# Kernel tuning notes

Hardware: AMD Instinct MI355X
Metric: run time of the kernel (lower is better)

## Reference

```python
import jax, jax.numpy as jnp
import numpy as np

KERNEL = 8


def setup_inputs() -> dict:
    key = jax.random.key(0)
    ks = jax.random.split(key, 9)
    N, Cin, L = 16, 128, 2048
    Cout = 256
    x = jax.random.normal(ks[0], (N, Cin, L), dtype=jnp.float32)
    conv_w = jax.random.normal(ks[1], (Cout, Cin, KERNEL), dtype=jnp.float32) * (1.0 / np.sqrt(Cin * KERNEL))
    conv_b = jax.random.normal(ks[2], (Cout,), dtype=jnp.float32) * 0.01
    wq = jax.random.normal(ks[3], (Cout, Cout), dtype=jnp.float32) * (1.0 / np.sqrt(Cout))
    bq = jax.random.normal(ks[4], (Cout,), dtype=jnp.float32) * 0.01
    wk = jax.random.normal(ks[5], (Cout, Cout), dtype=jnp.float32) * (1.0 / np.sqrt(Cout))
    bk = jax.random.normal(ks[6], (Cout,), dtype=jnp.float32) * 0.01
    wv = jax.random.normal(ks[7], (Cout, Cout), dtype=jnp.float32) * (1.0 / np.sqrt(Cout))
    bv = jax.random.normal(ks[8], (Cout,), dtype=jnp.float32) * 0.01
    return {"x": x, "conv_w": conv_w, "conv_b": conv_b,
            "wq": wq, "bq": bq, "wk": wk, "bk": bk, "wv": wv, "bv": bv}


def reference(x, conv_w, conv_b, wq, bq, wk, bk, wv, bv):
    # Conv1d, valid padding: [N, Cin, L] -> [N, Cout, S], S = L - KERNEL + 1
    h = jax.lax.conv_general_dilated(
        x, conv_w, window_strides=(1,), padding='VALID',
        dimension_numbers=('NCH', 'OIH', 'NCH'))
    h = jax.nn.relu(h + conv_b[None, :, None])
    N, C, S = h.shape
    h = jnp.transpose(h, (0, 2, 1))  # [N, S, C]
    # Linear layers (torch convention: y = x @ W^T + b)
    q = jnp.einsum('nsc,dc->nsd', h, wq) + bq
    k = jnp.einsum('nsc,dc->nsd', h, wk) + bk
    v = jnp.einsum('nsc,dc->nsd', h, wv) + bv
    # sigmoid (non-normalized) attention over full SxS scores
    scores = jnp.einsum('nsd,ntd->nst', q, k) / jnp.sqrt(jnp.asarray(C, h.dtype))
    attn = jax.nn.sigmoid(scores)  # [N, S, S]
    out = jnp.einsum('nst,ntd->nsd', attn, v)
    return jnp.transpose(out, (0, 2, 1))  # [N, C, S]
```

## Files before the change

kernel.cpp:

```cpp
#include <hip/hip_runtime.h>

typedef short short8 __attribute__((ext_vector_type(8)));
typedef float f32x4 __attribute__((ext_vector_type(4)));
typedef float f32x16 __attribute__((ext_vector_type(16)));
typedef unsigned short u16x4 __attribute__((ext_vector_type(4)));

constexpr int NB = 16, CIN = 128, LIN = 2048, CO = 256;
constexpr int SL = 2041;
constexpr int MP = 32768;
constexpr int XTS = 136;
constexpr int QSTR = 2048 * CO + 256;


constexpr size_t XT_OFF = 0;
constexpr size_t XT_SZ  = (size_t)NB*LIN*XTS*2 + 65536;
constexpr size_t CW_OFF = XT_OFF + XT_SZ;
constexpr size_t CW_SZ  = (size_t)CO*CIN*8*2;
constexpr size_t WQ_OFF = CW_OFF + CW_SZ;
constexpr size_t WB_SZ  = (size_t)CO*CO*2;
constexpr size_t WK_OFF = WQ_OFF + WB_SZ;
constexpr size_t WV_OFF = WK_OFF + WB_SZ;
constexpr size_t Q_OFF  = WV_OFF + WB_SZ;
constexpr size_t QK_SZ  = (size_t)NB*QSTR*2 + 256;
constexpr size_t K_OFF  = Q_OFF + QK_SZ;
constexpr size_t VT_OFF = K_OFF + QK_SZ;

__device__ inline unsigned short f2bf(float f) {
  union { float f; unsigned int u; } v; v.f = f;
  unsigned int r = v.u + 0x7fffu + ((v.u >> 16) & 1u);
  return (unsigned short)(r >> 16);
}

__device__ inline void sync_lds() {
  __asm__ volatile("" ::: "memory");
  __builtin_amdgcn_s_waitcnt(0xc07f);
  __builtin_amdgcn_s_barrier();
  __asm__ volatile("" ::: "memory");
}
__device__ inline void barrier_only() {
  __asm__ volatile("" ::: "memory");
  __builtin_amdgcn_s_barrier();
  __asm__ volatile("" ::: "memory");
}

#if defined(__has_builtin)
#if __has_builtin(__builtin_amdgcn_global_load_lds)
#define HAVE_GLDS 1
#endif
#endif

__device__ inline void gld16(const unsigned short* g, void* l) {
#ifdef HAVE_GLDS
  __builtin_amdgcn_global_load_lds(
      (const __attribute__((address_space(1))) void*)g,
      (__attribute__((address_space(3))) void*)l, 16, 0, 0);
#else
  *(short8*)l = *(const short8*)g;
#endif
}

__global__ __launch_bounds__(256) void prep_kernel(
    const float* __restrict__ x, unsigned short* __restrict__ xt,
    const float* __restrict__ cw_in, unsigned short* __restrict__ cw_out,
    const float* __restrict__ wq, const float* __restrict__ wk, const float* __restrict__ wv,
    unsigned short* __restrict__ wqb, unsigned short* __restrict__ wkb,
    unsigned short* __restrict__ wvb) {
  __shared__ float tile[32][33];
  const int b = blockIdx.x;
  const int tid = threadIdx.x;
  if (b < 4096) {
    const int tx = tid & 31, ty = tid >> 5;
    const int s0 = (b & 63) * 32, c0 = ((b >> 6) & 3) * 32, n = b >> 8;
    #pragma unroll
    for (int r = 0; r < 4; ++r)
      tile[ty * 4 + r][tx] = x[((size_t)(n * CIN + c0 + ty * 4 + r)) * LIN + s0 + tx];
    __syncthreads();
    #pragma unroll
    for (int r = 0; r < 4; ++r)
      xt[((size_t)(n * LIN + s0 + ty * 4 + r)) * XTS + c0 + tx] = f2bf(tile[tx][ty * 4 + r]);
  } else if (b < 4096 + 1024) {
    int idx = (b - 4096) * 256 + tid;
    int co = idx >> 10, r = idx & 1023, kp = r >> 7, ci = r & 127;
    cw_out[idx] = f2bf(cw_in[co * 1024 + ci * 8 + kp]);
  } else {
    int lb2 = b - (4096 + 1024);
    int z = lb2 >> 6, lb = lb2 & 63;
    const float* src = (z == 0) ? wq : (z == 1) ? wk : wv;
    unsigned short* dst = (z == 0) ? wqb : (z == 1) ? wkb : wvb;
    int i = (lb * 256 + tid) * 4;
    float4 v = *(const float4*)(src + i);
    u16x4 r;
    r.x = f2bf(v.x); r.y = f2bf(v.y); r.z = f2bf(v.z); r.w = f2bf(v.w);
    *(u16x4*)(dst + i) = r;
  }
}

__global__ __launch_bounds__(256, 2) void conv_qkv(
    const unsigned short* __restrict__ xt,
    const unsigned short* __restrict__ wb,
    const float* __restrict__ cbias,
    const unsigned short* __restrict__ Bq, const unsigned short* __restrict__ Bk,
    const unsigned short* __restrict__ Bv,
    const float* __restrict__ biq, const float* __restrict__ bik,
    const float* __restrict__ biv,
    unsigned short* __restrict__ qb, unsigned short* __restrict__ kb,
    unsigned short* __restrict__ vtb)
{
  __shared__ unsigned short regA[16384];
  __shared__ unsigned short sB[2][8192];
  unsigned short* const sX = regA;
  unsigned short* const hL = regA;
  const int tid = threadIdx.x;
  const int w = tid >> 6, lane = tid & 63, quad = lane >> 4, l16 = lane & 15;
  const int sg = w >> 1, dh = w & 1;
  const int n = blockIdx.y, s0 = blockIdx.x * 64;

  {
    const unsigned short* xbase = xt + ((size_t)n * LIN + s0) * XTS;
    #pragma unroll
    for (int i = 0; i < 5; ++i) {
      int u = i * 256 + tid;
      if (u < 1207) gld16(xbase + u * 8, ((char*)sX) + u * 16);
    }
  }

  const int brow0 = tid >> 2, bkgs = tid & 3;
  short8 breg[4];
  #pragma unroll
  for (int i2 = 0; i2 < 4; ++i2) {
    int row = i2 * 64 + brow0;
    int kg = bkgs ^ ((row >> 1) & 3);
    breg[i2] = *(const short8*)(wb + (size_t)row * 1024 + kg * 8);
  }
  #pragma unroll
  for (int i2 = 0; i2 < 4; ++i2)
    *(short8*)(&sB[0][(i2 * 256 + tid) * 8]) = breg[i2];
  __syncthreads();

  f32x4 acc[2][8];
  #pragma unroll
  for (int i = 0; i < 2; ++i)
    #pragma unroll
    for (int j = 0; j < 8; ++j) acc[i][j] = (f32x4){0.f, 0.f, 0.f, 0.f};

  for (int kc = 0; kc < 32; ++kc) {
    const int kcn = (kc < 31) ? kc + 1 : kc;
    const int kpn = kcn >> 2, ci0n = (kcn & 3) * 32;
    #pragma unroll
    for (int i2 = 0; i2 < 4; ++i2) {
      int row = i2 * 64 + brow0;
      int kg = bkgs ^ ((row >> 1) & 3);
      breg[i2] = *(const short8*)(wb + (size_t)row * 1024 + kpn * 128 + ci0n + kg * 8);
    }

    const int kp = kc >> 2, ci0 = (kc & 3) * 32;
    const unsigned short* sBc = sB[kc & 1];
    short8 bfr[8];
    #pragma unroll
    for (int j = 0; j < 8; ++j) {
      int r = dh * 128 + j * 16 + l16;
      bfr[j] = *(const short8*)(sBc + r * 32 + (quad ^ ((r >> 1) & 3)) * 8);
    }
    #pragma unroll
    for (int i = 0; i < 2; ++i) {
      int srow = sg * 32 + i * 16 + l16;
      short8 afr = *(const short8*)(sX + (srow + kp) * XTS + ci0 + quad * 8);
      #pragma unroll
      for (int j = 0; j < 8; ++j)
        acc[i][j] = __builtin_amdgcn_mfma_f32_16x16x32_bf16(afr, bfr[j], acc[i][j], 0, 0, 0);
    }

    #pragma unroll
    for (int i2 = 0; i2 < 4; ++i2)
      *(short8*)(&sB[(kc + 1) & 1][(i2 * 256 + tid) * 8]) = breg[i2];
    sync_lds();
  }

  #pragma unroll
  for (int i = 0; i < 2; ++i)
    #pragma unroll
    for (int j = 0; j < 8; ++j) {
      int c = dh * 128 + j * 16 + l16;
      float bv = cbias[c];
      int cc = (c >> 5) * 32 + (c & 7);
      int g = (c >> 3) & 3;
      #pragma unroll
      for (int jj = 0; jj < 4; ++jj) {
        int r = sg * 32 + i * 16 + quad * 4 + jj;
        hL[r * 256 + cc + ((g ^ ((r >> 1) & 3)) << 3)] =
            f2bf(fmaxf(acc[i][j][jj] + bv, 0.f));
      }
    }

  for (int z = 0; z < 3; ++z) {
    const unsigned short* B = (z == 0) ? Bq : (z == 1) ? Bk : Bv;
    const float* bias        = (z == 0) ? biq : (z == 1) ? bik : biv;

    #pragma unroll
    for (int i2 = 0; i2 < 4; ++i2) {
      int row = i2 * 64 + brow0;
      int kg = bkgs ^ ((row >> 1) & 3);
      breg[i2] = *(const short8*)(B + (size_t)row * CO + kg * 8);
    }
    #pragma unroll
    for (int i2 = 0; i2 < 4; ++i2)
      *(short8*)(&sB[0][(i2 * 256 + tid) * 8]) = breg[i2];
    sync_lds();

    #pragma unroll
    for (int i = 0; i < 2; ++i)
      #pragma unroll
      for (int j = 0; j < 8; ++j) acc[i][j] = (f32x4){0.f, 0.f, 0.f, 0.f};

    for (int kc = 0; kc < 8; ++kc) {
      const int kcn = (kc < 7) ? kc + 1 : kc;
      #pragma unroll
      for (int i2 = 0; i2 < 4; ++i2) {
        int row = i2 * 64 + brow0;
        int kg = bkgs ^ ((row >> 1) & 3);
        breg[i2] = *(const short8*)(B + (size_t)row * CO + kcn * 32 + kg * 8);
      }

      const unsigned short* sBc = sB[kc & 1];
      short8 afr[2], bfr[8];
      #pragma unroll
      for (int i = 0; i < 2; ++i) {
        int r = sg * 32 + i * 16 + l16;
        afr[i] = *(const short8*)(hL + r * 256 + kc * 32 + ((quad ^ ((r >> 1) & 3)) << 3));
      }
      #pragma unroll
      for (int j = 0; j < 8; ++j) {
        int r = dh * 128 + j * 16 + l16;
        bfr[j] = *(const short8*)(sBc + r * 32 + (quad ^ ((r >> 1) & 3)) * 8);
      }
      #pragma unroll
      for (int i = 0; i < 2; ++i)
        #pragma unroll
        for (int j = 0; j < 8; ++j)
          acc[i][j] = __builtin_amdgcn_mfma_f32_16x16x32_bf16(afr[i], bfr[j], acc[i][j], 0, 0, 0);

      #pragma unroll
      for (int i2 = 0; i2 < 4; ++i2)
        *(short8*)(&sB[(kc + 1) & 1][(i2 * 256 + tid) * 8]) = breg[i2];
      sync_lds();
    }

    if (z < 2) {
      unsigned short* base = ((z == 0) ? qb : kb) + (size_t)n * QSTR + (size_t)s0 * CO;
      #pragma unroll
      for (int i = 0; i < 2; ++i)
        #pragma unroll
        for (int j = 0; j < 8; ++j) {
          int c = dh * 128 + j * 16 + l16;
          float bv = bias[c];
          #pragma unroll
          for (int jj = 0; jj < 4; ++jj) {
            int r = sg * 32 + i * 16 + quad * 4 + jj;
            base[(size_t)r * CO + c] = f2bf(acc[i][j][jj] + bv);
          }
        }
    } else {
      #pragma unroll
      for (int i = 0; i < 2; ++i)
        #pragma unroll
        for (int j = 0; j < 8; ++j) {
          int c = dh * 128 + j * 16 + l16;
          float bv = bias[c];
          int mb = sg * 32 + i * 16 + quad * 4;
          u16x4 pk;
          #pragma unroll
          for (int jj = 0; jj < 4; ++jj) pk[jj] = f2bf(acc[i][j][jj] + bv);
          *(u16x4*)(hL + c * 64 + (mb ^ ((c & 7) << 3))) = pk;
        }
      sync_lds();
      const int c = tid;
      unsigned short* vrow = vtb + (size_t)c * MP + n * 2048 + s0;
      #pragma unroll
      for (int b = 0; b < 8; ++b) {
        int ml = b * 8;
        int ss = s0 + ml;
        short8 val = *(const short8*)(hL + c * 64 + (ml ^ ((c & 7) << 3)));
        if (ss + 7 >= SL) {
          #pragma unroll
          for (int e = 0; e < 8; ++e)
            if (ss + e >= SL) val[e] = 0;
        }
        *(short8*)(vrow + ml) = val;
      }
    }
  }
}

__global__ __launch_bounds__(512, 2) void attn_kernel(
    const unsigned short* __restrict__ qb,
    const unsigned short* __restrict__ kb,
    const unsigned short* __restrict__ vtb,
    float* __restrict__ out)
{
  __shared__ unsigned short sK[2][16384];
  __shared__ unsigned short sV[2][16384];
  __shared__ unsigned short sP[8192];
  const int tid = threadIdx.x;
  const int w = tid >> 6, lane = tid & 63;
  const int half = lane >> 5, l32 = lane & 31;
  const int bidx = blockIdx.x;
  const int n = (bidx & 7) + ((bidx >> 7) << 3);
  const int s0 = ((bidx >> 3) & 15) * 128;
  const int sr = w & 3, tr = w >> 2;

  const unsigned short* kbN = kb + (size_t)n * QSTR;
  const unsigned short* vbN = vtb + (size_t)n * 2048;

#define STAGE_TILE(buf, tk)                                                      \
  {                                                                              \
    _Pragma("unroll")                                                            \
    for (int i = 0; i < 4; ++i) {                                                \
      int u = i * 512 + tid;                                                     \
      int t = u >> 5, sl = u & 31;                                               \
      gld16(kbN + (size_t)((tk) + t) * CO + ((sl ^ (t & 31)) << 3),              \
            ((char*)sK[buf]) + u * 16);                                          \
    }                                                                            \
    _Pragma("unroll")                                                            \
    for (int i = 0; i < 4; ++i) {                                                \
      int u = i * 512 + tid;                                                     \
      int d = u >> 3, sl = u & 7;                                                \
      gld16(vbN + (size_t)d * MP + (tk) + ((sl ^ (d & 7)) << 3),                 \
            ((char*)sV[buf]) + u * 16);                                          \
    }                                                                            \
  }

  STAGE_TILE(0, 0)

  short8 qf[16];
  {
    const unsigned short* qp = qb + (size_t)n * QSTR
                             + (size_t)(s0 + sr * 32 + l32) * CO + half * 8;
    #pragma unroll
    for (int kk = 0; kk < 16; ++kk) qf[kk] = *(const short8*)(qp + kk * 16);
  }

  __builtin_amdgcn_s_waitcnt(0x0F70);
  barrier_only();

  f32x16 o[4];
  #pragma unroll
  for (int di = 0; di < 4; ++di)
    #pragma unroll
    for (int r = 0; r < 16; ++r) o[di][r] = 0.f;

  for (int it = 0; it < 32; ++it) {
    const int cur = it & 1;
    if (it < 31) {
      STAGE_TILE(cur ^ 1, (it + 1) * 64)
      __builtin_amdgcn_s_waitcnt(0x0F78);
    } else {
      __builtin_amdgcn_s_waitcnt(0x0F70);
    }
    barrier_only();

    const unsigned short* sKc = sK[cur];
    const int tl = tr * 32 + l32;
    f32x16 sacc;
    #pragma unroll
    for (int r = 0; r < 16; ++r) sacc[r] = 0.f;
    #pragma unroll
    for (int kk = 0; kk < 16; ++kk) {
      short8 kf = *(const short8*)(sKc + tl * 256 + (((kk * 2 + half) ^ (tl & 31)) << 3));
      sacc = __builtin_amdgcn_mfma_f32_32x32x16_bf16(kf, qf[kk], sacc, 0, 0, 0);
    }

    const int t0 = it * 64;
    #pragma unroll
    for (int q2 = 0; q2 < 4; ++q2) {
      u16x4 pk;
      #pragma unroll
      for (int e = 0; e < 4; ++e) {
        int tg = t0 + tr * 32 + 8 * q2 + 4 * half + e;
        float p = __builtin_amdgcn_rcpf(1.f + __expf(-sacc[q2 * 4 + e] * 0.0625f));
        pk[e] = (tg < SL) ? f2bf(p) : (unsigned short)0;
      }
      *(u16x4*)(sP + ((tr * 4 + q2) * 128 + sr * 32 + l32) * 8 + 4 * half) = pk;
    }
    sync_lds();

    const unsigned short* sVc = sV[cur];
    #pragma unroll
    for (int kt = 0; kt < 4; ++kt) {
      int g = kt * 2 + half;
      short8 pa = *(const short8*)(sP + ((g << 7) + sr * 32 + l32) * 8);
      #pragma unroll
      for (int di = 0; di < 4; ++di) {
        int d = tr * 128 + di * 32 + l32;
        short8 vf = *(const short8*)(sVc + d * 64 + ((g ^ (d & 7)) << 3));
        o[di] = __builtin_amdgcn_mfma_f32_32x32x16_bf16(vf, pa, o[di], 0, 0, 0);
      }
    }
    sync_lds();
  }

  const int s = s0 + sr * 32 + l32;
  if (s < SL) {
    float* op = out + (size_t)n * CO * SL + s;
    #pragma unroll
    for (int di = 0; di < 4; ++di)
      #pragma unroll
      for (int r = 0; r < 16; ++r) {
        int d = tr * 128 + di * 32 + (r & 3) + 8 * (r >> 2) + 4 * half;
        __builtin_nontemporal_store(o[di][r], op + (size_t)d * SL);
      }
  }
#undef STAGE_TILE
}

extern "C" void kernel_launch(void* const* d_in, const int* in_sizes, int n_in,
                              void* d_out, int out_size, void* d_ws, size_t ws_size,
                              hipStream_t stream) {
  const float* x      = (const float*)d_in[0];
  const float* conv_w = (const float*)d_in[1];
  const float* conv_b = (const float*)d_in[2];
  const float* wq     = (const float*)d_in[3];
  const float* bq     = (const float*)d_in[4];
  const float* wk     = (const float*)d_in[5];
  const float* bk     = (const float*)d_in[6];
  const float* wv     = (const float*)d_in[7];
  const float* bv     = (const float*)d_in[8];

  char* ws = (char*)d_ws;
  unsigned short* xt  = (unsigned short*)(ws + XT_OFF);
  unsigned short* cw  = (unsigned short*)(ws + CW_OFF);
  unsigned short* wqb = (unsigned short*)(ws + WQ_OFF);
  unsigned short* wkb = (unsigned short*)(ws + WK_OFF);
  unsigned short* wvb = (unsigned short*)(ws + WV_OFF);
  unsigned short* qb  = (unsigned short*)(ws + Q_OFF);
  unsigned short* kb  = (unsigned short*)(ws + K_OFF);
  unsigned short* vtb = (unsigned short*)(ws + VT_OFF);

  hipLaunchKernelGGL(prep_kernel, dim3(4096 + 1024 + 192), dim3(256), 0, stream,
                     x, xt, conv_w, cw, wq, wk, wv, wqb, wkb, wvb);
  hipLaunchKernelGGL(conv_qkv, dim3(32, 16), dim3(256), 0, stream,
                     xt, cw, conv_b, wqb, wkb, wvb, bq, bk, bv, qb, kb, vtb);
  hipLaunchKernelGGL(attn_kernel, dim3(256), dim3(512), 0, stream,
                     qb, kb, vtb, (float*)d_out);
}
```

Baseline: 231.8 us.

## Load conv and QKV weight fragments directly from global memory, dropping LDS staging

The conv_qkv kernel stops staging weight tiles through a double-buffered LDS array and instead has each wave read its B-fragments straight from global memory (expected to be L2-resident). This removes the per-iteration LDS writes and block barriers, and frees 32 KB of shared memory, which could allow higher occupancy. In exchange, every wave issues redundant global loads with no prefetch, so the MFMA loop may stall on global latency. Extra barriers are added around the reuse of the shared h buffer.

Result: slower. 286.6 us (+23.7%).

```diff
diff --git a/kernel.cpp b/kernel.cpp
--- a/kernel.cpp
+++ b/kernel.cpp
@@ -107,7 +107,6 @@
     unsigned short* __restrict__ vtb)
 {
   __shared__ unsigned short regA[16384];
-  __shared__ unsigned short sB[2][8192];
   unsigned short* const sX = regA;
   unsigned short* const hL = regA;
   const int tid = threadIdx.x;
@@ -123,18 +122,6 @@
       if (u < 1207) gld16(xbase + u * 8, ((char*)sX) + u * 16);
     }
   }
-
-  const int brow0 = tid >> 2, bkgs = tid & 3;
-  short8 breg[4];
-  #pragma unroll
-  for (int i2 = 0; i2 < 4; ++i2) {
-    int row = i2 * 64 + brow0;
-    int kg = bkgs ^ ((row >> 1) & 3);
-    breg[i2] = *(const short8*)(wb + (size_t)row * 1024 + kg * 8);
-  }
-  #pragma unroll
-  for (int i2 = 0; i2 < 4; ++i2)
-    *(short8*)(&sB[0][(i2 * 256 + tid) * 8]) = breg[i2];
   __syncthreads();
 
   f32x4 acc[2][8];
@@ -144,22 +131,13 @@
     for (int j = 0; j < 8; ++j) acc[i][j] = (f32x4){0.f, 0.f, 0.f, 0.f};
 
   for (int kc = 0; kc < 32; ++kc) {
-    const int kcn = (kc < 31) ? kc + 1 : kc;
-    const int kpn = kcn >> 2, ci0n = (kcn & 3) * 32;
-    #pragma unroll
-    for (int i2 = 0; i2 < 4; ++i2) {
-      int row = i2 * 64 + brow0;
-      int kg = bkgs ^ ((row >> 1) & 3);
-      breg[i2] = *(const short8*)(wb + (size_t)row * 1024 + kpn * 128 + ci0n + kg * 8);
-    }
-
     const int kp = kc >> 2, ci0 = (kc & 3) * 32;
-    const unsigned short* sBc = sB[kc & 1];
+    const unsigned short* wcol = wb + kp * 128 + ci0 + quad * 8;
     short8 bfr[8];
     #pragma unroll
     for (int j = 0; j < 8; ++j) {
-      int r = dh * 128 + j * 16 + l16;
-      bfr[j] = *(const short8*)(sBc + r * 32 + (quad ^ ((r >> 1) & 3)) * 8);
+      int row = dh * 128 + j * 16 + l16;
+      bfr[j] = *(const short8*)(wcol + (size_t)row * 1024);
     }
     #pragma unroll
     for (int i = 0; i < 2; ++i) {
@@ -169,12 +147,9 @@
       for (int j = 0; j < 8; ++j)
         acc[i][j] = __builtin_amdgcn_mfma_f32_16x16x32_bf16(afr, bfr[j], acc[i][j], 0, 0, 0);
     }
-
-    #pragma unroll
-    for (int i2 = 0; i2 < 4; ++i2)
-      *(short8*)(&sB[(kc + 1) & 1][(i2 * 256 + tid) * 8]) = breg[i2];
-    sync_lds();
-  }
+  }
+
+  sync_lds();
 
   #pragma unroll
   for (int i = 0; i < 2; ++i)
@@ -191,58 +166,35 @@
             f2bf(fmaxf(acc[i][j][jj] + bv, 0.f));
       }
     }
+  sync_lds();
 
   for (int z = 0; z < 3; ++z) {
     const unsigned short* B = (z == 0) ? Bq : (z == 1) ? Bk : Bv;
     const float* bias        = (z == 0) ? biq : (z == 1) ? bik : biv;
 
     #pragma unroll
-    for (int i2 = 0; i2 < 4; ++i2) {
-      int row = i2 * 64 + brow0;
-      int kg = bkgs ^ ((row >> 1) & 3);
-      breg[i2] = *(const short8*)(B + (size_t)row * CO + kg * 8);
-    }
-    #pragma unroll
-    for (int i2 = 0; i2 < 4; ++i2)
-      *(short8*)(&sB[0][(i2 * 256 + tid) * 8]) = breg[i2];
-    sync_lds();
-
-    #pragma unroll
     for (int i = 0; i < 2; ++i)
       #pragma unroll
       for (int j = 0; j < 8; ++j) acc[i][j] = (f32x4){0.f, 0.f, 0.f, 0.f};
 
     for (int kc = 0; kc < 8; ++kc) {
-      const int kcn = (kc < 7) ? kc + 1 : kc;
-      #pragma unroll
-      for (int i2 = 0; i2 < 4; ++i2) {
-        int row = i2 * 64 + brow0;
-        int kg = bkgs ^ ((row >> 1) & 3);
-        breg[i2] = *(const short8*)(B + (size_t)row * CO + kcn * 32 + kg * 8);
-      }
-
-      const unsigned short* sBc = sB[kc & 1];
-      short8 afr[2], bfr[8];
+      short8 bfr[8];
+      #pragma unroll
+      for (int j = 0; j < 8; ++j) {
+        int row = dh * 128 + j * 16 + l16;
+        bfr[j] = *(const short8*)(B + (size_t)row * CO + kc * 32 + quad * 8);
+      }
+      short8 afr[2];
       #pragma unroll
       for (int i = 0; i < 2; ++i) {
         int r = sg * 32 + i * 16 + l16;
         afr[i] = *(const short8*)(hL + r * 256 + kc * 32 + ((quad ^ ((r >> 1) & 3)) << 3));
-      }
-      #pragma unroll
-      for (int j = 0; j < 8; ++j) {
-        int r = dh * 128 + j * 16 + l16;
-        bfr[j] = *(const short8*)(sBc + r * 32 + (quad ^ ((r >> 1) & 3)) * 8);
       }
       #pragma unroll
       for (int i = 0; i < 2; ++i)
         #pragma unroll
         for (int j = 0; j < 8; ++j)
           acc[i][j] = __builtin_amdgcn_mfma_f32_16x16x32_bf16(afr[i], bfr[j], acc[i][j], 0, 0, 0);
-
-      #pragma unroll
-      for (int i2 = 0; i2 < 4; ++i2)
-        *(short8*)(&sB[(kc + 1) & 1][(i2 * 256 + tid) * 8]) = breg[i2];
-      sync_lds();
     }
 
     if (z < 2) {
@@ -260,6 +212,7 @@
           }
         }
     } else {
+      sync_lds();
       #pragma unroll
       for (int i = 0; i < 2; ++i)
         #pragma unroll
```
